# Performance work log

Hardware: AMD Instinct MI355X
Metric: run time of the kernel (lower is better)

## Reference

```python
import jax, jax.numpy as jnp
import numpy as np

B, H_TRAJ, S = 8, 16, 64
DIM, C = 128, 2000
D = 2 * DIM            # transformer d_model
NUM_HEADS, WINDOW, L = 4, 4, 2
D_FF = 4 * D


def setup_inputs() -> dict:
    key = jax.random.key(0)
    ks = jax.random.split(key, 12)
    w = lambda k, shape, s: jax.random.normal(k, shape, jnp.float32) * s
    return {
        "history": jax.random.randint(ks[0], (B, H_TRAJ, S), 0, C + 1),
        "current_trajectory": jax.random.randint(ks[1], (B, S), 0, C + 1),
        "embedding": w(ks[2], (1, C, DIM), 1.0),
        "null_embedding": jax.random.uniform(ks[3], (D,), jnp.float32),
        "gcn_w": w(ks[4], (DIM, DIM), 0.05),
        "gcn_b": jnp.zeros((DIM,), jnp.float32),
        "enc_attn_w": w(ks[5], (L, 4, D, D), 0.05),
        "enc_attn_b": jnp.zeros((L, 4, D), jnp.float32),
        "enc_ffn_w1": w(ks[6], (L, D, D_FF), 0.05),
        "enc_ffn_b1": jnp.zeros((L, D_FF), jnp.float32),
        "enc_ffn_w2": w(ks[7], (L, D_FF, D), 0.05),
        "enc_ffn_b2": jnp.zeros((L, D), jnp.float32),
        "enc_ln_s": jnp.ones((L, 2, D), jnp.float32),
        "enc_ln_b": jnp.zeros((L, 2, D), jnp.float32),
        "wca_w": w(ks[8], (4, D, D), 0.05),
        "wca_b": jnp.zeros((4, D), jnp.float32),
        "ial_w": w(ks[9], (D, DIM), 0.05),
        "ial_b": jnp.zeros((DIM,), jnp.float32),
    }


def _layer_norm(x, s, b, eps=1e-5):
    m = x.mean(-1, keepdims=True)
    v = ((x - m) ** 2).mean(-1, keepdims=True)
    return (x - m) * jax.lax.rsqrt(v + eps) * s + b


def _mha(xq, xkv, w, b, mask):
    # w: (4,d,d) q/k/v/out, b: (4,d); mask additive, broadcast over heads
    d = xq.shape[-1]
    hd = d // NUM_HEADS
    proj = lambda x, i: (x @ w[i] + b[i]).reshape(x.shape[:-1] + (NUM_HEADS, hd))
    q, k, v = proj(xq, 0), proj(xkv, 1), proj(xkv, 2)
    s = jnp.einsum('bqhd,bkhd->bhqk', q, k) / float(np.sqrt(hd))
    s = s + mask[:, None, :, :]
    a = jax.nn.softmax(s, axis=-1)
    o = jnp.einsum('bhqk,bkhd->bqhd', a, v).reshape(xq.shape)
    return o @ w[3] + b[3]


def _get_graph(history):
    # vectorized scatter-add replacement of the python triple loop
    src, dst = history[:, :, :-1], history[:, :, 1:]
    h_idx = jnp.arange(H_TRAJ, dtype=jnp.float32)
    wts = 1.0 + jnp.exp(-0.01 * (H_TRAJ - 1 - h_idx))          # per-trajectory weight
    valid = (src != C) & (dst != C) & (src != dst)
    wv = jnp.where(valid, wts[None, :, None], 0.0)
    sc, dc = jnp.clip(src, 0, C - 1), jnp.clip(dst, 0, C - 1)
    flat = (jnp.arange(B)[:, None, None] * C * C + sc * C + dc).ravel()
    A = jnp.zeros((B * C * C,), jnp.float32).at[flat].add(wv.ravel())
    return A.reshape(B, C, C)


def _mytransform(A):
    A = A + jnp.eye(C, dtype=A.dtype)
    d = jnp.sqrt(A.sum(axis=1))          # torch code: sqrt of dim-1 sums (no inverse)
    return d[:, :, None] * A * d[:, None, :]   # D @ A @ D


def _temporal(seq_len, d):
    t = jnp.arange(seq_len, dtype=jnp.float32)[:, None]
    den = 10000.0 ** (jnp.arange(0, d, 2, dtype=jnp.float32) / d)
    arg = t / den[None, :]
    return jnp.stack([jnp.sin(arg), jnp.cos(arg)], axis=-1).reshape(seq_len, d)


def _fuse(pos, hist, temp, null_emb):
    # pos: (B,C,D); hist: (B,...,S); gather + where fusion
    g = jax.vmap(lambda p, h: p[h])(pos, jnp.clip(hist, 0, C - 1))
    return jnp.where((hist == C)[..., None], null_emb + temp, g + temp)


def _encoder(x, mask, aw, ab, fw1, fb1, fw2, fb2, lns, lnb):
    for l in range(L):
        a = _mha(x, x, aw[l], ab[l], mask)
        x = _layer_norm(x + a, lns[l, 0], lnb[l, 0])
        f = jax.nn.relu(x @ fw1[l] + fb1[l]) @ fw2[l] + fb2[l]
        x = _layer_norm(x + f, lns[l, 1], lnb[l, 1])
    return x


def reference(history, current_trajectory, embedding, null_embedding, gcn_w, gcn_b,
              enc_attn_w, enc_attn_b, enc_ffn_w1, enc_ffn_b1, enc_ffn_w2, enc_ffn_b2,
              enc_ln_s, enc_ln_b, wca_w, wca_b, ial_w, ial_b):
    E = jnp.broadcast_to(embedding, (B, C, DIM))
    A = _mytransform(_get_graph(history))                      # (B,C,C)
    Eg = jax.nn.relu(A @ E @ gcn_w + gcn_b)                    # GCN layer
    pos = jnp.concatenate([E, Eg], axis=-1)                    # (B,C,2*dim)
    temp = _temporal(S, D)
    fh = _fuse(pos, history, temp, null_embedding).reshape(B * H_TRAJ, S, D)
    fc = _fuse(pos, current_trajectory, temp, null_embedding)  # (B,S,D)
    hmask = jnp.broadcast_to(
        jnp.where((history == C)[:, :, None, :], -jnp.inf, 0.0),
        (B, H_TRAJ, S, S)).reshape(B * H_TRAJ, S, S)
    cmask = jnp.broadcast_to(
        jnp.where((current_trajectory == C)[:, None, :], -jnp.inf, 0.0), (B, S, S))
    mh = _encoder(fh, hmask, enc_attn_w, enc_attn_b, enc_ffn_w1, enc_ffn_b1,
                  enc_ffn_w2, enc_ffn_b2, enc_ln_s, enc_ln_b)
    mc = _encoder(fc, cmask, enc_attn_w, enc_attn_b, enc_ffn_w1, enc_ffn_b1,
                  enc_ffn_w2, enc_ffn_b2, enc_ln_s, enc_ln_b)
    cur_rep = jnp.broadcast_to(mc[:, None], (B, H_TRAJ, S, D)).reshape(B * H_TRAJ, S, D)
    i = jnp.arange(S)
    wmask = jnp.where(jnp.abs(i[:, None] - i[None, :]) <= WINDOW, 0.0, -jnp.inf)[None]
    wca = mh + _mha(mh, cur_rep, wca_w, wca_b, wmask)          # window-based cross attn
    wca = wca.reshape(B, H_TRAJ, S, D)
    # information aggregation over the trajectory axis
    scores = jnp.einsum('bhsd,bsd->bhs', wca, mc) / float(np.sqrt(D))
    aw = jax.nn.softmax(scores, axis=1)
    agg = jnp.einsum('bhs,bhsd->bsd', aw, wca)
    final = jax.nn.relu((agg + mc) @ ial_w + ial_b)            # (B,S,dim)
    return final @ embedding[0].T                              # (B,S,C)
```

## Files before the change

kernel.cpp:

```cpp
#include <hip/hip_runtime.h>
#include <hip/hip_bf16.h>
#include <math.h>

#define C_N   2000
#define DIMN  128
#define DM    256
#define B_N   8
#define HT    16
#define S_N   64
#define NSEQ  136
#define DFF   1024
#define NEDGE (B_N*HT*(S_N-1))

typedef __hip_bfloat16 bf16;
typedef short bf16x8 __attribute__((ext_vector_type(8)));
typedef float f32x4  __attribute__((ext_vector_type(4)));

#define GLOAD_LDS16(gp, lp) \
    __builtin_amdgcn_global_load_lds((const __attribute__((address_space(1))) void*)(gp), \
                                     (__attribute__((address_space(3))) void*)(lp), 16, 0, 0)

__device__ __forceinline__ short f2bf(float v) {
    bf16 t = (bf16)v;
    return *reinterpret_cast<short*>(&t);
}


__global__ void k_initX(const float* __restrict__ cs, const float* __restrict__ Y,
                        const float* __restrict__ gb, float* __restrict__ Eg) {
    size_t i = (size_t)blockIdx.x * 256 + threadIdx.x;
    int k = (int)(i % DIMN); size_t bc = i / DIMN;
    int c = (int)(bc % C_N); int b = (int)(bc / C_N);
    float dd2 = 1.f + cs[b * C_N + c];
    Eg[i] = dd2 * Y[(size_t)c * DIMN + k] + gb[k];
}

__global__ void k_edgeX(const int* __restrict__ hist, const float* __restrict__ cs,
                        const float* __restrict__ Y, float* __restrict__ Eg) {
    int e = blockIdx.x;
    int s = e % (S_N-1); int bh = e / (S_N-1); int h = bh % HT; int b = bh / HT;
    const int* row = hist + (size_t)bh * S_N;
    int src = row[s], dst = row[s+1];
    if (src == C_N || dst == C_N || src == dst) return;
    float w = (1.f + expf(-0.01f * (float)(HT - 1 - h)))
            * sqrtf(1.f + cs[b*C_N+src]) * sqrtf(1.f + cs[b*C_N+dst]);
    int k = threadIdx.x;
    atomicAdd(&Eg[((size_t)b * C_N + src) * DIMN + k], w * Y[(size_t)dst * DIMN + k]);
}

struct TEnt { const float* s; bf16* d; int K; int N; int nm; int tiles; };
struct PrepArgs {
    TEnt e[6];
    const float* emb; bf16* embbf;
    const int* hist; float* colsum;
    float* temp;
};

__global__ void k_prep(PrepArgs p) {
    int id = blockIdx.x;
    int t = threadIdx.y * 32 + threadIdx.x;
    if (id < 1840) {
        __shared__ float tl[32][33];
        TEnt en = p.e[0];
        #pragma unroll
        for (int k = 0; k < 6; ++k) {
            if (id < p.e[k].tiles) { en = p.e[k]; break; }
            id -= p.e[k].tiles;
        }
        int tn = en.N >> 5;
        int per = (en.K >> 5) * tn;
        int mat = id / per, t2 = id % per;
        int ty = t2 / tn, tx = t2 % tn;
        const float* s = en.s + (size_t)mat * en.K * en.N;
        bf16* d = en.d + (size_t)mat * en.N * en.K;
        int k0 = ty * 32, n0 = tx * 32;
        #pragma unroll
        for (int j = 0; j < 32; j += 8)
            tl[threadIdx.y + j][threadIdx.x] = s[(size_t)(k0 + threadIdx.y + j) * en.N + n0 + threadIdx.x];
        __syncthreads();
        #pragma unroll
        for (int j = 0; j < 32; j += 8)
            d[(size_t)(n0 + threadIdx.y + j) * en.K + k0 + threadIdx.x] = (bf16)tl[threadIdx.x][threadIdx.y + j];
        return;
    }
    id -= 1840;
    if (id < 250) {
        int i = (id * 256 + t) * 4;
        float4 v = *(const float4*)(p.emb + i);
        bf16* d = p.embbf;
        d[i] = (bf16)v.x; d[i+1] = (bf16)v.y; d[i+2] = (bf16)v.z; d[i+3] = (bf16)v.w;
        return;
    }
    id -= 250;
    if (id < 32) {
        int e = id * 256 + t;
        if (e >= NEDGE) return;
        int s = e % (S_N-1); int bh = e / (S_N-1); int h = bh % HT; int b = bh / HT;
        const int* row = p.hist + (size_t)bh * S_N;
        int src = row[s], dst = row[s+1];
        if (src != C_N && dst != C_N && src != dst) {
            float w = 1.f + expf(-0.01f * (float)(HT - 1 - h));
            atomicAdd(&p.colsum[b * C_N + dst], w);
        }
        return;
    }
    id -= 32;
    {
        int s = id; int d = t;
        int k = d >> 1;
        float den = powf(10000.f, (2.f * (float)k) / 256.f);
        float arg = (float)s / den;
        p.temp[s * DM + d] = (d & 1) ? cosf(arg) : sinf(arg);
    }
}

template<int EPI>
__global__ __launch_bounds__(256) void k_bgemm(
        const bf16* __restrict__ A, const bf16* __restrict__ Bt,
        const float* __restrict__ bias, const float* __restrict__ resid,
        void* __restrict__ Cout, int M, int N, int K, int ldc, int nreal)
{
    __shared__ bf16 As[2][128 * 64];
    __shared__ bf16 Bs[2][64 * 64];
    int tid = threadIdx.x;
    int wid = tid >> 6, lane = tid & 63;
    int m0 = blockIdx.y * 128, n0 = blockIdx.x * 64;
    int wr = wid >> 1, wc = wid & 1;
    int lr = lane >> 3, lc = lane & 7;
    int gc = lc ^ lr;
    f32x4 acc[4][2] = {};
    int nkt = K >> 6;

#define STAGE_BG(kt, buf) { \
    int kb = (kt) << 6; \
    _Pragma("unroll") \
    for (int s = 0; s < 4; ++s) { \
        int seg = wid * 4 + s; int row = seg * 8 + lr; \
        GLOAD_LDS16(A + (size_t)(m0 + row) * K + kb + gc * 8, &As[buf][seg * 512]); \
    } \
    _Pragma("unroll") \
    for (int s = 0; s < 2; ++s) { \
        int seg = wid * 2 + s; int row = seg * 8 + lr; \
        GLOAD_LDS16(Bt + (size_t)(n0 + row) * K + kb + gc * 8, &Bs[buf][seg * 512]); \
    } }

    STAGE_BG(0, 0);
    __syncthreads();
    int cur = 0;
    for (int kt = 0; kt < nkt; ++kt) {
        if (kt + 1 < nkt) STAGE_BG(kt + 1, cur ^ 1);
        #pragma unroll
        for (int kk = 0; kk < 2; ++kk) {
            bf16x8 af[4], bfr[2];
            int c = kk * 4 + (lane >> 4);
            #pragma unroll
            for (int m = 0; m < 4; ++m) {
                int row = wr * 64 + m * 16 + (lane & 15);
                af[m] = *(const bf16x8*)(&As[cur][row * 64 + (c ^ (row & 7)) * 8]);
            }
            #pragma unroll
            for (int n = 0; n < 2; ++n) {
                int row = wc * 32 + n * 16 + (lane & 15);
                bfr[n] = *(const bf16x8*)(&Bs[cur][row * 64 + (c ^ (row & 7)) * 8]);
            }
            #pragma unroll
            for (int m = 0; m < 4; ++m)
                #pragma unroll
                for (int n = 0; n < 2; ++n)
                    acc[m][n] = __builtin_amdgcn_mfma_f32_16x16x32_bf16(af[m], bfr[n], acc[m][n], 0, 0, 0);
        }
        __syncthreads();
        cur ^= 1;
    }
#undef STAGE_BG
    int cl = lane & 15, ch = lane >> 4;
    #pragma unroll
    for (int n = 0; n < 2; ++n) {
        int col = n0 + wc * 32 + n * 16 + cl;
        if ((EPI & 16) && col >= nreal) continue;
        float bv = (EPI & 1) ? bias[col] : 0.f;
        #pragma unroll
        for (int m = 0; m < 4; ++m) {
            #pragma unroll
            for (int j = 0; j < 4; ++j) {
                int row = m0 + wr * 64 + m * 16 + ch * 4 + j;
                float v = acc[m][n][j] + bv;
                if (EPI & 4) v += resid[(size_t)row * ldc + col];
                if (EPI & 2) v = fmaxf(v, 0.f);
                if (EPI & 8) ((bf16*)Cout)[(size_t)row * ldc + col] = (bf16)v;
                else         ((float*)Cout)[(size_t)row * ldc + col] = v;
            }
        }
    }
}

__global__ __launch_bounds__(256) void k_bgemm_ln(
        const bf16* __restrict__ A, const bf16* __restrict__ Bt,
        const float* __restrict__ bias, float* __restrict__ Xf,
        const float* __restrict__ lns_, const float* __restrict__ lnb_,
        bf16* __restrict__ Xb, int M, int K)
{
    __shared__ bf16 As[2][32 * 64];
    __shared__ bf16 Bs[2][256 * 64];
    __shared__ float ls1[32][4], ls2[32][4];
    int tid = threadIdx.x, wid = tid >> 6, lane = tid & 63;
    int lr = lane >> 3, lc = lane & 7, gc = lc ^ lr;
    int cl = lane & 15, ch = lane >> 4;
    int m0 = blockIdx.x * 32;
    int wc = wid;
    f32x4 acc[2][4] = {};
    int nkt = K >> 6;

#define STAGE_LN(kt, buf) { \
    int kb = (kt) << 6; \
    { int row = wid * 8 + lr; \
      GLOAD_LDS16(A + (size_t)(m0 + row) * K + kb + gc * 8, &As[buf][wid * 512]); } \
    _Pragma("unroll") \
    for (int s = 0; s < 8; ++s) { \
        int seg = wid * 8 + s; int row = seg * 8 + lr; \
        GLOAD_LDS16(Bt + (size_t)row * K + kb + gc * 8, &Bs[buf][seg * 512]); \
    } }

    STAGE_LN(0, 0);
    __syncthreads();
    int cur = 0;
    for (int kt = 0; kt < nkt; ++kt) {
        if (kt + 1 < nkt) STAGE_LN(kt + 1, cur ^ 1);
        #pragma unroll
        for (int kk = 0; kk < 2; ++kk) {
            int c = kk * 4 + ch;
            bf16x8 af[2], bfr[4];
            #pragma unroll
            for (int m = 0; m < 2; ++m) {
                int row = m * 16 + cl;
                af[m] = *(const bf16x8*)(&As[cur][row * 64 + (c ^ (row & 7)) * 8]);
            }
            #pragma unroll
            for (int n = 0; n < 4; ++n) {
                int row = wc * 64 + n * 16 + cl;
                bfr[n] = *(const bf16x8*)(&Bs[cur][row * 64 + (c ^ (row & 7)) * 8]);
            }
            #pragma unroll
            for (int m = 0; m < 2; ++m)
                #pragma unroll
                for (int n = 0; n < 4; ++n)
                    acc[m][n] = __builtin_amdgcn_mfma_f32_16x16x32_bf16(af[m], bfr[n], acc[m][n], 0, 0, 0);
        }
        __syncthreads();
        cur ^= 1;
    }
#undef STAGE_LN
    #pragma unroll
    for (int m = 0; m < 2; ++m) {
        #pragma unroll
        for (int j = 0; j < 4; ++j) {
            int rl = m * 16 + ch * 4 + j;
            float s1 = 0.f, s2 = 0.f;
            #pragma unroll
            for (int n = 0; n < 4; ++n) {
                int col = wc * 64 + n * 16 + cl;
                float v = acc[m][n][j] + bias[col] + Xf[(size_t)(m0 + rl) * 256 + col];
                acc[m][n][j] = v;
                s1 += v; s2 += v * v;
            }
            s1 += __shfl_xor(s1, 1); s2 += __shfl_xor(s2, 1);
            s1 += __shfl_xor(s1, 2); s2 += __shfl_xor(s2, 2);
            s1 += __shfl_xor(s1, 4); s2 += __shfl_xor(s2, 4);
            s1 += __shfl_xor(s1, 8); s2 += __shfl_xor(s2, 8);
            if (cl == 0) { ls1[rl][wc] = s1; ls2[rl][wc] = s2; }
        }
    }
    __syncthreads();
    #pragma unroll
    for (int m = 0; m < 2; ++m) {
        #pragma unroll
        for (int j = 0; j < 4; ++j) {
            int rl = m * 16 + ch * 4 + j;
            float su = ls1[rl][0] + ls1[rl][1] + ls1[rl][2] + ls1[rl][3];
            float sq = ls2[rl][0] + ls2[rl][1] + ls2[rl][2] + ls2[rl][3];
            float mean = su * (1.f / 256.f);
            float var  = sq * (1.f / 256.f) - mean * mean;
            float rstd = rsqrtf(var + 1e-5f);
            #pragma unroll
            for (int n = 0; n < 4; ++n) {
                int col = wc * 64 + n * 16 + cl;
                float r = (acc[m][n][j] - mean) * rstd * lns_[col] + lnb_[col];
                size_t g = (size_t)(m0 + rl) * 256 + col;
                Xf[g] = r;
                Xb[g] = (bf16)r;
            }
        }
    }
}


__global__ void k_fuse(const int* __restrict__ hist, const int* __restrict__ cur,
                       const float* __restrict__ E, const float* __restrict__ Eg,
                       const float* __restrict__ nullE, const float* __restrict__ temp,
                       float* __restrict__ Xenc, bf16* __restrict__ Xbf,
                       float* __restrict__ maskb) {
    int blk = blockIdx.x;
    int seq = blk >> 6, s = blk & 63;
    int d = threadIdx.x;
    int idx, b;
    if (seq < 128) { b = seq >> 4; idx = hist[(size_t)seq * S_N + s]; }
    else           { b = seq - 128; idx = cur[b * S_N + s]; }
    float t = temp[s * DM + d];
    float v;
    if (idx == C_N) v = nullE[d] + t;
    else {
        v = ((d < DIMN) ? E[(size_t)idx * DIMN + d]
                        : fmaxf(Eg[((size_t)b * C_N + idx) * DIMN + (d - DIMN)], 0.f)) + t;
    }
    size_t o = ((size_t)seq * S_N + s) * DM + d;
    Xenc[o] = v;
    Xbf[o]  = (bf16)v;
    if (d == 0) maskb[seq * S_N + s] = (idx == C_N) ? -INFINITY : 0.f;
}

template<bool WCA>
__global__ __launch_bounds__(64) void k_mattn(
        const bf16* __restrict__ Qb, const bf16* __restrict__ Kb,
        const bf16* __restrict__ Vb, const float* __restrict__ maskb,
        bf16* __restrict__ O, int qstr, int kstr)
{
    int seq = blockIdx.x >> 2, head = blockIdx.x & 3;
    int lane = threadIdx.x;
    int cl = lane & 15, ch = lane >> 4;
    __shared__ __align__(16) short VT[64 * 72];
    __shared__ __align__(16) short PT[64 * 72];

    const bf16* Qp = Qb + (size_t)seq * 64 * qstr + head * 64;
    int kvseq = WCA ? (seq >> 4) : seq;
    const bf16* Kp = Kb + (size_t)kvseq * 64 * kstr + head * 64;
    const bf16* Vp = Vb + (size_t)kvseq * 64 * kstr + head * 64;

    bf16x8 aq[4][2], bk[4][2], vr[4][2];
    #pragma unroll
    for (int t = 0; t < 4; ++t)
        #pragma unroll
        for (int kk = 0; kk < 2; ++kk) {
            int row = t * 16 + cl, d0 = kk * 32 + ch * 8;
            aq[t][kk] = *(const bf16x8*)(Qp + (size_t)row * qstr + d0);
            bk[t][kk] = *(const bf16x8*)(Kp + (size_t)row * kstr + d0);
            vr[t][kk] = *(const bf16x8*)(Vp + (size_t)row * kstr + d0);
        }

    f32x4 sa[4][4] = {};
    #pragma unroll
    for (int kk = 0; kk < 2; ++kk)
        #pragma unroll
        for (int m = 0; m < 4; ++m)
            #pragma unroll
            for (int n = 0; n < 4; ++n)
                sa[m][n] = __builtin_amdgcn_mfma_f32_16x16x32_bf16(aq[m][kk], bk[n][kk], sa[m][n], 0, 0, 0);

    #pragma unroll
    for (int t = 0; t < 4; ++t)
        #pragma unroll
        for (int kk = 0; kk < 2; ++kk) {
            int k = t * 16 + cl, d0 = kk * 32 + ch * 8;
            #pragma unroll
            for (int e = 0; e < 8; ++e)
                VT[(d0 + e) * 72 + k] = vr[t][kk][e];
        }

    float mk4[4];
    if (!WCA) {
        #pragma unroll
        for (int n = 0; n < 4; ++n) mk4[n] = maskb[seq * 64 + n * 16 + cl];
    }

    #pragma unroll
    for (int m = 0; m < 4; ++m) {
        #pragma unroll
        for (int j = 0; j < 4; ++j) {
            int q = m * 16 + ch * 4 + j;
            float rm = -INFINITY;
            #pragma unroll
            for (int n = 0; n < 4; ++n) {
                int k = n * 16 + cl;
                float msk = WCA ? ((abs(q - k) <= 4) ? 0.f : -INFINITY) : mk4[n];
                float v = sa[m][n][j] * 0.125f + msk;
                sa[m][n][j] = v;
                rm = fmaxf(rm, v);
            }
            rm = fmaxf(rm, __shfl_xor(rm, 1));
            rm = fmaxf(rm, __shfl_xor(rm, 2));
            rm = fmaxf(rm, __shfl_xor(rm, 4));
            rm = fmaxf(rm, __shfl_xor(rm, 8));
            float rs = 0.f;
            #pragma unroll
            for (int n = 0; n < 4; ++n) {
                float e = expf(sa[m][n][j] - rm);
                sa[m][n][j] = e;
                rs += e;
            }
            rs += __shfl_xor(rs, 1);
            rs += __shfl_xor(rs, 2);
            rs += __shfl_xor(rs, 4);
            rs += __shfl_xor(rs, 8);
            float inv = 1.f / rs;
            #pragma unroll
            for (int n = 0; n < 4; ++n)
                PT[q * 72 + n * 16 + cl] = f2bf(sa[m][n][j] * inv);
        }
    }
    __syncthreads();

    f32x4 oa[4][4] = {};
    #pragma unroll
    for (int kk = 0; kk < 2; ++kk) {
        bf16x8 av[4], bp[4];
        #pragma unroll
        for (int dm = 0; dm < 4; ++dm)
            av[dm] = *(const bf16x8*)(VT + (dm * 16 + cl) * 72 + kk * 32 + ch * 8);
        #pragma unroll
        for (int qn = 0; qn < 4; ++qn)
            bp[qn] = *(const bf16x8*)(PT + (qn * 16 + cl) * 72 + kk * 32 + ch * 8);
        #pragma unroll
        for (int dm = 0; dm < 4; ++dm)
            #pragma unroll
            for (int qn = 0; qn < 4; ++qn)
                oa[dm][qn] = __builtin_amdgcn_mfma_f32_16x16x32_bf16(av[dm], bp[qn], oa[dm][qn], 0, 0, 0);
    }
    __syncthreads();

    #pragma unroll
    for (int dm = 0; dm < 4; ++dm)
        #pragma unroll
        for (int qn = 0; qn < 4; ++qn)
            #pragma unroll
            for (int j = 0; j < 4; ++j)
                PT[(qn * 16 + cl) * 72 + dm * 16 + ch * 4 + j] = f2bf(oa[dm][qn][j]);
    __syncthreads();
    #pragma unroll
    for (int it = 0; it < 8; ++it) {
        int chunk = it * 64 + lane;
        int tok = chunk >> 3, d0 = (chunk & 7) * 8;
        bf16x8 v = *(const bf16x8*)(PT + tok * 72 + d0);
        *(bf16x8*)(O + ((size_t)seq * 64 + tok) * 256 + head * 64 + d0) = v;
    }
}


__global__ __launch_bounds__(256) void k_agg(const float* __restrict__ wca,
                                             const float* __restrict__ mc,
                                             bf16* __restrict__ aggbf) {
    int bs = blockIdx.x; int b = bs >> 6, s = bs & 63;
    int d = threadIdx.x;
    __shared__ float red[4][16];
    float mcv = mc[((size_t)b * S_N + s) * DM + d];
    float wv[16], p[16];
    #pragma unroll
    for (int h = 0; h < 16; ++h) {
        wv[h] = wca[(((size_t)(b * HT + h)) * S_N + s) * DM + d];
        p[h] = wv[h] * mcv;
    }
    #pragma unroll
    for (int o = 1; o < 64; o <<= 1)
        #pragma unroll
        for (int h = 0; h < 16; ++h) p[h] += __shfl_xor(p[h], o);
    if ((d & 63) == 0) {
        int w = d >> 6;
        #pragma unroll
        for (int h = 0; h < 16; ++h) red[w][h] = p[h];
    }
    __syncthreads();
    float sc[16], mx = -INFINITY;
    #pragma unroll
    for (int h = 0; h < 16; ++h) {
        sc[h] = (red[0][h] + red[1][h] + red[2][h] + red[3][h]) * (1.f / 16.f);
        mx = fmaxf(mx, sc[h]);
    }
    float e[16], sum = 0.f;
    #pragma unroll
    for (int h = 0; h < 16; ++h) { e[h] = expf(sc[h] - mx); sum += e[h]; }
    float inv = 1.f / sum;
    float acc = 0.f;
    #pragma unroll
    for (int h = 0; h < 16; ++h) acc += e[h] * inv * wv[h];
    aggbf[((size_t)b * S_N + s) * DM + d] = (bf16)(acc + mcv);
}


extern "C" void kernel_launch(void* const* d_in, const int* in_sizes, int n_in,
                              void* d_out, int out_size, void* d_ws, size_t ws_size,
                              hipStream_t stream) {
    const int*   history = (const int*)d_in[0];
    const int*   cur     = (const int*)d_in[1];
    const float* emb     = (const float*)d_in[2];
    const float* nullE   = (const float*)d_in[3];
    const float* gcn_w   = (const float*)d_in[4];
    const float* gcn_b   = (const float*)d_in[5];
    const float* aw      = (const float*)d_in[6];
    const float* ab      = (const float*)d_in[7];
    const float* fw1     = (const float*)d_in[8];
    const float* fb1     = (const float*)d_in[9];
    const float* fw2     = (const float*)d_in[10];
    const float* fb2     = (const float*)d_in[11];
    const float* lns     = (const float*)d_in[12];
    const float* lnb     = (const float*)d_in[13];
    const float* wca_w   = (const float*)d_in[14];
    const float* wca_b   = (const float*)d_in[15];
    const float* ial_w   = (const float*)d_in[16];
    const float* ial_b   = (const float*)d_in[17];
    float* out = (float*)d_out;
    float* ws  = (float*)d_ws;

    float* dvec   = ws + 0;
    float* maskb  = ws + 16000;
    float* temp   = ws + 24704;
    bf16*  aggbf  = (bf16*)(ws + 41088);
    bf16*  finalb = (bf16*)(ws + 106624);
    bf16*  embbf  = (bf16*)(ws + 139392);
    float* Y      = ws + 270464;
    float* Eg     = ws + 532608;
    bf16*  wbf    = (bf16*)(ws + 2580608);
    float* Xenc   = ws + 3522688;
    bf16*  Xbf    = (bf16*)(ws + 5750912);
    bf16*  Abf    = (bf16*)(ws + 6865024);
    bf16*  Hbf    = (bf16*)(ws + 7979136);
    bf16*  QKVbf  = (bf16*)(ws + 12435584);
    float* SE     = ws + 15777920;

    bf16* wbf_aw  = wbf;
    bf16* wbf_fw1 = wbf + 524288;
    bf16* wbf_fw2 = wbf + 1048576;
    bf16* wbf_wca = wbf + 1572864;
    bf16* wbf_gcn = wbf + 1835008;
    bf16* wbf_ial = wbf + 1851392;

    bf16* Qwbf = QKVbf;
    bf16* KVbf = QKVbf + 4194304;

    hipMemsetAsync(dvec, 0, 16000 * sizeof(float), stream);
    hipMemsetAsync(embbf + 2000 * 128, 0, 48 * 128 * sizeof(bf16), stream);
    PrepArgs pa;
    pa.e[0] = { aw,    wbf_aw,  256,  256, 8, 512 };
    pa.e[1] = { fw1,   wbf_fw1, 256, 1024, 2, 512 };
    pa.e[2] = { fw2,   wbf_fw2, 1024, 256, 2, 512 };
    pa.e[3] = { wca_w, wbf_wca, 256,  256, 4, 256 };
    pa.e[4] = { gcn_w, wbf_gcn, 128,  128, 1,  16 };
    pa.e[5] = { ial_w, wbf_ial, 256,  128, 1,  32 };
    pa.emb = emb; pa.embbf = embbf;
    pa.hist = history; pa.colsum = dvec;
    pa.temp = temp;
    k_prep<<<1840 + 250 + 32 + 64, dim3(32, 8), 0, stream>>>(pa);

    k_bgemm<0><<<dim3(2, 16), 256, 0, stream>>>(embbf, wbf_gcn, nullptr, nullptr, Y,
                                                2048, DIMN, DIMN, DIMN, DIMN);
    k_initX<<<B_N * C_N * DIMN / 256, 256, 0, stream>>>(dvec, Y, gcn_b, Eg);
    k_edgeX<<<NEDGE, 128, 0, stream>>>(history, dvec, Y, Eg);

    k_fuse<<<NSEQ * S_N, DM, 0, stream>>>(history, cur, emb, Eg, nullE, temp, Xenc, Xbf, maskb);

    for (int l = 0; l < 2; ++l) {
        k_bgemm<9><<<dim3(12, 68), 256, 0, stream>>>(Xbf, wbf_aw + l * 262144,
                ab + l * 1024, nullptr, QKVbf, NSEQ * S_N, 768, 256, 768, 768);
        k_mattn<false><<<NSEQ * 4, 64, 0, stream>>>(QKVbf, QKVbf + 256, QKVbf + 512,
                maskb, Abf, 768, 768);
        k_bgemm_ln<<<272, 256, 0, stream>>>(Abf, wbf_aw + l * 262144 + 196608,
                ab + l * 1024 + 768, Xenc, lns + (l * 2 + 0) * DM, lnb + (l * 2 + 0) * DM,
                Xbf, NSEQ * S_N, 256);
        k_bgemm<11><<<dim3(16, 68), 256, 0, stream>>>(Xbf, wbf_fw1 + l * 262144,
                fb1 + l * DFF, nullptr, Hbf, NSEQ * S_N, DFF, 256, DFF, DFF);
        k_bgemm_ln<<<272, 256, 0, stream>>>(Hbf, wbf_fw2 + l * 262144,
                fb2 + l * DM, Xenc, lns + (l * 2 + 1) * DM, lnb + (l * 2 + 1) * DM,
                Xbf, NSEQ * S_N, 1024);
    }

    float* mh = Xenc;
    bf16*  mc_bf = Xbf + (size_t)128 * S_N * DM;

    k_bgemm<9><<<dim3(4, 64), 256, 0, stream>>>(Xbf, wbf_wca, wca_b, nullptr, Qwbf,
                                                128 * S_N, 256, 256, 256, 256);
    k_bgemm<9><<<dim3(8, 4), 256, 0, stream>>>(mc_bf, wbf_wca + 65536, wca_b + 256, nullptr,
                                               KVbf, B_N * S_N, 512, 256, 512, 512);
    k_mattn<true><<<128 * 4, 64, 0, stream>>>(Qwbf, KVbf, KVbf + 256, nullptr, Abf, 256, 512);
    k_bgemm<5><<<dim3(4, 64), 256, 0, stream>>>(Abf, wbf_wca + 196608, wca_b + 768, mh, SE,
                                                128 * S_N, 256, 256, 256, 256);

    k_agg<<<B_N * S_N, 256, 0, stream>>>(SE, Xenc + (size_t)128 * S_N * DM, aggbf);
    k_bgemm<11><<<dim3(2, 4), 256, 0, stream>>>(aggbf, wbf_ial, ial_b, nullptr, finalb,
                                                B_N * S_N, DIMN, DM, DIMN, DIMN);
    k_bgemm<16><<<dim3(32, 4), 256, 0, stream>>>(finalb, embbf, nullptr, nullptr, out,
                                                 B_N * S_N, 2048, DIMN, C_N, C_N);
}
```

Baseline: 320.7 us.

## Fuse attention with output projection and LayerNorm, widen GEMM tiles to 128x128

Attention now runs one block per sequence with four head warps. The per-head outputs are staged in LDS and multiplied directly by the output-projection weight, followed by the residual add and LayerNorm (or, for the window cross-attention, the residual write into SE). This removes the Abf round trip and one GEMM launch per layer. The generic GEMM tile grows from 128x64 to 128x128, and the cross-attention Q and KV projections are merged into one launch. The trade-off is fewer blocks per launch (136 or 128 for attention) with more LDS per block, so occupancy and parallelism drop.

```diff
diff --git a/kernel.cpp b/kernel.cpp
--- a/kernel.cpp
+++ b/kernel.cpp
@@ -11,6 +11,7 @@
 #define NSEQ  136
 #define DFF   1024
 #define NEDGE (B_N*HT*(S_N-1))
+#define OTS   264
 
 typedef __hip_bfloat16 bf16;
 typedef short bf16x8 __attribute__((ext_vector_type(8)));
@@ -115,68 +116,66 @@
 }
 
 template<int EPI>
-__global__ __launch_bounds__(256) void k_bgemm(
+__device__ __forceinline__ void bgemm2_body(
         const bf16* __restrict__ A, const bf16* __restrict__ Bt,
-        const float* __restrict__ bias, const float* __restrict__ resid,
-        void* __restrict__ Cout, int M, int N, int K, int ldc, int nreal)
+        const float* __restrict__ bias, void* __restrict__ Cout,
+        int m0, int n0, int K, int ldc, int nreal,
+        bf16* __restrict__ As, bf16* __restrict__ Bs)
 {
-    __shared__ bf16 As[2][128 * 64];
-    __shared__ bf16 Bs[2][64 * 64];
     int tid = threadIdx.x;
     int wid = tid >> 6, lane = tid & 63;
-    int m0 = blockIdx.y * 128, n0 = blockIdx.x * 64;
     int wr = wid >> 1, wc = wid & 1;
     int lr = lane >> 3, lc = lane & 7;
     int gc = lc ^ lr;
-    f32x4 acc[4][2] = {};
+    f32x4 acc[4][4] = {};
     int nkt = K >> 6;
 
-#define STAGE_BG(kt, buf) { \
+#define STAGE2(kt, buf) { \
     int kb = (kt) << 6; \
     _Pragma("unroll") \
     for (int s = 0; s < 4; ++s) { \
         int seg = wid * 4 + s; int row = seg * 8 + lr; \
-        GLOAD_LDS16(A + (size_t)(m0 + row) * K + kb + gc * 8, &As[buf][seg * 512]); \
+        GLOAD_LDS16(A + (size_t)(m0 + row) * K + kb + gc * 8, As + (buf) * 8192 + seg * 512); \
     } \
     _Pragma("unroll") \
-    for (int s = 0; s < 2; ++s) { \
-        int seg = wid * 2 + s; int row = seg * 8 + lr; \
-        GLOAD_LDS16(Bt + (size_t)(n0 + row) * K + kb + gc * 8, &Bs[buf][seg * 512]); \
+    for (int s = 0; s < 4; ++s) { \
+        int seg = wid * 4 + s; int row = seg * 8 + lr; \
+        GLOAD_LDS16(Bt + (size_t)(n0 + row) * K + kb + gc * 8, Bs + (buf) * 8192 + seg * 512); \
     } }
 
-    STAGE_BG(0, 0);
+    STAGE2(0, 0);
     __syncthreads();
     int cur = 0;
     for (int kt = 0; kt < nkt; ++kt) {
-        if (kt + 1 < nkt) STAGE_BG(kt + 1, cur ^ 1);
+        if (kt + 1 < nkt) STAGE2(kt + 1, cur ^ 1);
         #pragma unroll
         for (int kk = 0; kk < 2; ++kk) {
-            bf16x8 af[4], bfr[2];
+            bf16x8 af[4], bfr[4];
             int c = kk * 4 + (lane >> 4);
             #pragma unroll
             for (int m = 0; m < 4; ++m) {
                 int row = wr * 64 + m * 16 + (lane & 15);
-                af[m] = *(const bf16x8*)(&As[cur][row * 64 + (c ^ (row & 7)) * 8]);
-            }
-            #pragma unroll
-            for (int n = 0; n < 2; ++n) {
-                int row = wc * 32 + n * 16 + (lane & 15);
-                bfr[n] = *(const bf16x8*)(&Bs[cur][row * 64 + (c ^ (row & 7)) * 8]);
+                af[m] = *(const bf16x8*)(As + cur * 8192 + row * 64 + (c ^ (row & 7)) * 8);
+            }
+            #pragma unroll
+            for (int n = 0; n < 4; ++n) {
+                int row = wc * 64 + n * 16 + (lane & 15);
+                bfr[n] = *(const bf16x8*)(Bs + cur * 8192 + row * 64 + (c ^ (row & 7)) * 8);
             }
             #pragma unroll
             for (int m = 0; m < 4; ++m)
                 #pragma unroll
-                for (int n = 0; n < 2; ++n)
+                for (int n = 0; n < 4; ++n)
                     acc[m][n] = __builtin_amdgcn_mfma_f32_16x16x32_bf16(af[m], bfr[n], acc[m][n], 0, 0, 0);
         }
         __syncthreads();
         cur ^= 1;
     }
-#undef STAGE_BG
+#undef STAGE2
     int cl = lane & 15, ch = lane >> 4;
     #pragma unroll
-    for (int n = 0; n < 2; ++n) {
-        int col = n0 + wc * 32 + n * 16 + cl;
+    for (int n = 0; n < 4; ++n) {
+        int col = n0 + wc * 64 + n * 16 + cl;
         if ((EPI & 16) && col >= nreal) continue;
         float bv = (EPI & 1) ? bias[col] : 0.f;
         #pragma unroll
@@ -185,12 +184,39 @@
             for (int j = 0; j < 4; ++j) {
                 int row = m0 + wr * 64 + m * 16 + ch * 4 + j;
                 float v = acc[m][n][j] + bv;
-                if (EPI & 4) v += resid[(size_t)row * ldc + col];
                 if (EPI & 2) v = fmaxf(v, 0.f);
                 if (EPI & 8) ((bf16*)Cout)[(size_t)row * ldc + col] = (bf16)v;
                 else         ((float*)Cout)[(size_t)row * ldc + col] = v;
             }
         }
+    }
+}
+
+template<int EPI>
+__global__ __launch_bounds__(256) void k_bgemm2(
+        const bf16* __restrict__ A, const bf16* __restrict__ Bt,
+        const float* __restrict__ bias, void* __restrict__ Cout,
+        int K, int ldc, int nreal)
+{
+    __shared__ bf16 As[2][8192], Bs[2][8192];
+    bgemm2_body<EPI>(A, Bt, bias, Cout, blockIdx.y * 128, blockIdx.x * 128,
+                     K, ldc, nreal, &As[0][0], &Bs[0][0]);
+}
+
+__global__ __launch_bounds__(256) void k_wcaqkv(
+        const bf16* __restrict__ Xbf, const bf16* __restrict__ mcbf,
+        const bf16* __restrict__ wwca, const float* __restrict__ wb,
+        bf16* __restrict__ Q, bf16* __restrict__ KV)
+{
+    __shared__ bf16 As[2][8192], Bs[2][8192];
+    int bid = blockIdx.x;
+    if (bid < 128)
+        bgemm2_body<9>(Xbf, wwca, wb, Q, (bid >> 1) * 128, (bid & 1) * 128,
+                       256, 256, 0, &As[0][0], &Bs[0][0]);
+    else {
+        int l = bid - 128;
+        bgemm2_body<9>(mcbf, wwca + 65536, wb + 256, KV, (l >> 2) * 128, (l & 3) * 128,
+                       256, 512, 0, &As[0][0], &Bs[0][0]);
     }
 }
 
@@ -319,17 +345,28 @@
 }
 
 template<bool WCA>
-__global__ __launch_bounds__(64) void k_mattn(
+__global__ __launch_bounds__(256) void k_attnfuse(
         const bf16* __restrict__ Qb, const bf16* __restrict__ Kb,
         const bf16* __restrict__ Vb, const float* __restrict__ maskb,
-        bf16* __restrict__ O, int qstr, int kstr)
+        const bf16* __restrict__ Wt, const float* __restrict__ bias,
+        float* __restrict__ Xf, const float* __restrict__ lns_,
+        const float* __restrict__ lnb_, bf16* __restrict__ Xb,
+        float* __restrict__ SEout)
 {
-    int seq = blockIdx.x >> 2, head = blockIdx.x & 3;
-    int lane = threadIdx.x;
+    int seq = blockIdx.x;
+    int tid = threadIdx.x;
+    int wid = tid >> 6, lane = tid & 63;
+    int head = wid;
     int cl = lane & 15, ch = lane >> 4;
-    __shared__ __align__(16) short VT[64 * 72];
-    __shared__ __align__(16) short PT[64 * 72];
-
+    __shared__ __align__(16) short VTall[4][64 * 72];
+    __shared__ __align__(16) short PTall[4][64 * 72];
+    __shared__ __align__(16) short OT[64 * OTS];
+    __shared__ float ls1[64][4], ls2[64][4];
+    short* VT = VTall[wid];
+    short* PT = PTall[wid];
+
+    const int qstr = WCA ? 256 : 768;
+    const int kstr = WCA ? 512 : 768;
     const bf16* Qp = Qb + (size_t)seq * 64 * qstr + head * 64;
     int kvseq = WCA ? (seq >> 4) : seq;
     const bf16* Kp = Kb + (size_t)kvseq * 64 * kstr + head * 64;
@@ -345,7 +382,6 @@
             bk[t][kk] = *(const bf16x8*)(Kp + (size_t)row * kstr + d0);
             vr[t][kk] = *(const bf16x8*)(Vp + (size_t)row * kstr + d0);
         }
-
     f32x4 sa[4][4] = {};
     #pragma unroll
     for (int kk = 0; kk < 2; ++kk)
@@ -354,7 +390,6 @@
             #pragma unroll
             for (int n = 0; n < 4; ++n)
                 sa[m][n] = __builtin_amdgcn_mfma_f32_16x16x32_bf16(aq[m][kk], bk[n][kk], sa[m][n], 0, 0, 0);
-
     #pragma unroll
     for (int t = 0; t < 4; ++t)
         #pragma unroll
@@ -364,13 +399,11 @@
             for (int e = 0; e < 8; ++e)
                 VT[(d0 + e) * 72 + k] = vr[t][kk][e];
         }
-
     float mk4[4];
     if (!WCA) {
         #pragma unroll
         for (int n = 0; n < 4; ++n) mk4[n] = maskb[seq * 64 + n * 16 + cl];
     }
-
     #pragma unroll
     for (int m = 0; m < 4; ++m) {
         #pragma unroll
@@ -406,8 +439,6 @@
                 PT[q * 72 + n * 16 + cl] = f2bf(sa[m][n][j] * inv);
         }
     }
-    __syncthreads();
-
     f32x4 oa[4][4] = {};
     #pragma unroll
     for (int kk = 0; kk < 2; ++kk) {
@@ -424,22 +455,91 @@
             for (int qn = 0; qn < 4; ++qn)
                 oa[dm][qn] = __builtin_amdgcn_mfma_f32_16x16x32_bf16(av[dm], bp[qn], oa[dm][qn], 0, 0, 0);
     }
+    #pragma unroll
+    for (int dm = 0; dm < 4; ++dm)
+        #pragma unroll
+        for (int qn = 0; qn < 4; ++qn)
+            #pragma unroll
+            for (int j = 0; j < 4; ++j)
+                OT[(qn * 16 + cl) * OTS + head * 64 + dm * 16 + ch * 4 + j] = f2bf(oa[dm][qn][j]);
     __syncthreads();
 
-    #pragma unroll
-    for (int dm = 0; dm < 4; ++dm)
-        #pragma unroll
-        for (int qn = 0; qn < 4; ++qn)
-            #pragma unroll
-            for (int j = 0; j < 4; ++j)
-                PT[(qn * 16 + cl) * 72 + dm * 16 + ch * 4 + j] = f2bf(oa[dm][qn][j]);
+    f32x4 acc[4][4] = {};
+    #pragma unroll 2
+    for (int kt = 0; kt < 8; ++kt) {
+        int k0 = kt * 32 + ch * 8;
+        bf16x8 af[4], bfr[4];
+        #pragma unroll
+        for (int m = 0; m < 4; ++m)
+            af[m] = *(const bf16x8*)(OT + (m * 16 + cl) * OTS + k0);
+        #pragma unroll
+        for (int n = 0; n < 4; ++n) {
+            int col = wid * 64 + n * 16 + cl;
+            bfr[n] = *(const bf16x8*)(Wt + (size_t)col * 256 + k0);
+        }
+        #pragma unroll
+        for (int m = 0; m < 4; ++m)
+            #pragma unroll
+            for (int n = 0; n < 4; ++n)
+                acc[m][n] = __builtin_amdgcn_mfma_f32_16x16x32_bf16(af[m], bfr[n], acc[m][n], 0, 0, 0);
+    }
+
+    if (WCA) {
+        #pragma unroll
+        for (int m = 0; m < 4; ++m)
+            #pragma unroll
+            for (int j = 0; j < 4; ++j) {
+                int rl = m * 16 + ch * 4 + j;
+                size_t rb = ((size_t)seq * 64 + rl) * 256;
+                #pragma unroll
+                for (int n = 0; n < 4; ++n) {
+                    int col = wid * 64 + n * 16 + cl;
+                    SEout[rb + col] = acc[m][n][j] + bias[col] + Xf[rb + col];
+                }
+            }
+        return;
+    }
+    #pragma unroll
+    for (int m = 0; m < 4; ++m) {
+        #pragma unroll
+        for (int j = 0; j < 4; ++j) {
+            int rl = m * 16 + ch * 4 + j;
+            size_t rb = ((size_t)seq * 64 + rl) * 256;
+            float s1 = 0.f, s2 = 0.f;
+            #pragma unroll
+            for (int n = 0; n < 4; ++n) {
+                int col = wid * 64 + n * 16 + cl;
+                float v = acc[m][n][j] + bias[col] + Xf[rb + col];
+                acc[m][n][j] = v;
+                s1 += v; s2 += v * v;
+            }
+            s1 += __shfl_xor(s1, 1); s2 += __shfl_xor(s2, 1);
+            s1 += __shfl_xor(s1, 2); s2 += __shfl_xor(s2, 2);
+            s1 += __shfl_xor(s1, 4); s2 += __shfl_xor(s2, 4);
+            s1 += __shfl_xor(s1, 8); s2 += __shfl_xor(s2, 8);
+            if (cl == 0) { ls1[rl][wid] = s1; ls2[rl][wid] = s2; }
+        }
+    }
     __syncthreads();
     #pragma unroll
-    for (int it = 0; it < 8; ++it) {
-        int chunk = it * 64 + lane;
-        int tok = chunk >> 3, d0 = (chunk & 7) * 8;
-        bf16x8 v = *(const bf16x8*)(PT + tok * 72 + d0);
-        *(bf16x8*)(O + ((size_t)seq * 64 + tok) * 256 + head * 64 + d0) = v;
+    for (int m = 0; m < 4; ++m) {
+        #pragma unroll
+        for (int j = 0; j < 4; ++j) {
+            int rl = m * 16 + ch * 4 + j;
+            float su = ls1[rl][0] + ls1[rl][1] + ls1[rl][2] + ls1[rl][3];
+            float sq = ls2[rl][0] + ls2[rl][1] + ls2[rl][2] + ls2[rl][3];
+            float mean = su * (1.f / 256.f);
+            float var  = sq * (1.f / 256.f) - mean * mean;
+            float rstd = rsqrtf(var + 1e-5f);
+            size_t rb = ((size_t)seq * 64 + rl) * 256;
+            #pragma unroll
+            for (int n = 0; n < 4; ++n) {
+                int col = wid * 64 + n * 16 + cl;
+                float r = (acc[m][n][j] - mean) * rstd * lns_[col] + lnb_[col];
+                Xf[rb + col] = r;
+                Xb[rb + col] = (bf16)r;
+            }
+        }
     }
 }
 
@@ -519,10 +619,9 @@
     bf16*  wbf    = (bf16*)(ws + 2580608);
     float* Xenc   = ws + 3522688;
     bf16*  Xbf    = (bf16*)(ws + 5750912);
-    bf16*  Abf    = (bf16*)(ws + 6865024);
-    bf16*  Hbf    = (bf16*)(ws + 7979136);
-    bf16*  QKVbf  = (bf16*)(ws + 12435584);
-    float* SE     = ws + 15777920;
+    bf16*  Hbf    = (bf16*)(ws + 6865024);
+    bf16*  QKVbf  = (bf16*)(ws + 11321472);
+    float* SE     = ws + 14663808;
 
     bf16* wbf_aw  = wbf;
     bf16* wbf_fw1 = wbf + 524288;
@@ -548,23 +647,20 @@
     pa.temp = temp;
     k_prep<<<1840 + 250 + 32 + 64, dim3(32, 8), 0, stream>>>(pa);
 
-    k_bgemm<0><<<dim3(2, 16), 256, 0, stream>>>(embbf, wbf_gcn, nullptr, nullptr, Y,
-                                                2048, DIMN, DIMN, DIMN, DIMN);
+    k_bgemm2<0><<<dim3(1, 16), 256, 0, stream>>>(embbf, wbf_gcn, nullptr, Y, DIMN, DIMN, 0);
     k_initX<<<B_N * C_N * DIMN / 256, 256, 0, stream>>>(dvec, Y, gcn_b, Eg);
     k_edgeX<<<NEDGE, 128, 0, stream>>>(history, dvec, Y, Eg);
 
     k_fuse<<<NSEQ * S_N, DM, 0, stream>>>(history, cur, emb, Eg, nullE, temp, Xenc, Xbf, maskb);
 
     for (int l = 0; l < 2; ++l) {
-        k_bgemm<9><<<dim3(12, 68), 256, 0, stream>>>(Xbf, wbf_aw + l * 262144,
-                ab + l * 1024, nullptr, QKVbf, NSEQ * S_N, 768, 256, 768, 768);
-        k_mattn<false><<<NSEQ * 4, 64, 0, stream>>>(QKVbf, QKVbf + 256, QKVbf + 512,
-                maskb, Abf, 768, 768);
-        k_bgemm_ln<<<272, 256, 0, stream>>>(Abf, wbf_aw + l * 262144 + 196608,
-                ab + l * 1024 + 768, Xenc, lns + (l * 2 + 0) * DM, lnb + (l * 2 + 0) * DM,
-                Xbf, NSEQ * S_N, 256);
-        k_bgemm<11><<<dim3(16, 68), 256, 0, stream>>>(Xbf, wbf_fw1 + l * 262144,
-                fb1 + l * DFF, nullptr, Hbf, NSEQ * S_N, DFF, 256, DFF, DFF);
+        k_bgemm2<9><<<dim3(6, 68), 256, 0, stream>>>(Xbf, wbf_aw + l * 262144,
+                ab + l * 1024, QKVbf, 256, 768, 0);
+        k_attnfuse<false><<<NSEQ, 256, 0, stream>>>(QKVbf, QKVbf + 256, QKVbf + 512,
+                maskb, wbf_aw + l * 262144 + 196608, ab + l * 1024 + 768,
+                Xenc, lns + (l * 2 + 0) * DM, lnb + (l * 2 + 0) * DM, Xbf, nullptr);
+        k_bgemm2<11><<<dim3(8, 68), 256, 0, stream>>>(Xbf, wbf_fw1 + l * 262144,
+                fb1 + l * DFF, Hbf, 256, DFF, 0);
         k_bgemm_ln<<<272, 256, 0, stream>>>(Hbf, wbf_fw2 + l * 262144,
                 fb2 + l * DM, Xenc, lns + (l * 2 + 1) * DM, lnb + (l * 2 + 1) * DM,
                 Xbf, NSEQ * S_N, 1024);
@@ -573,17 +669,11 @@
     float* mh = Xenc;
     bf16*  mc_bf = Xbf + (size_t)128 * S_N * DM;
 
-    k_bgemm<9><<<dim3(4, 64), 256, 0, stream>>>(Xbf, wbf_wca, wca_b, nullptr, Qwbf,
-                                                128 * S_N, 256, 256, 256, 256);
-    k_bgemm<9><<<dim3(8, 4), 256, 0, stream>>>(mc_bf, wbf_wca + 65536, wca_b + 256, nullptr,
-                                               KVbf, B_N * S_N, 512, 256, 512, 512);
-    k_mattn<true><<<128 * 4, 64, 0, stream>>>(Qwbf, KVbf, KVbf + 256, nullptr, Abf, 256, 512);
-    k_bgemm<5><<<dim3(4, 64), 256, 0, stream>>>(Abf, wbf_wca + 196608, wca_b + 768, mh, SE,
-                                                128 * S_N, 256, 256, 256, 256);
+    k_wcaqkv<<<144, 256, 0, stream>>>(Xbf, mc_bf, wbf_wca, wca_b, Qwbf, KVbf);
+    k_attnfuse<true><<<128, 256, 0, stream>>>(Qwbf, KVbf, KVbf + 256, nullptr,
+            wbf_wca + 196608, wca_b + 768, mh, nullptr, nullptr, nullptr, SE);
 
     k_agg<<<B_N * S_N, 256, 0, stream>>>(SE, Xenc + (size_t)128 * S_N * DM, aggbf);
-    k_bgemm<11><<<dim3(2, 4), 256, 0, stream>>>(aggbf, wbf_ial, ial_b, nullptr, finalb,
-                                                B_N * S_N, DIMN, DM, DIMN, DIMN);
-    k_bgemm<16><<<dim3(32, 4), 256, 0, stream>>>(finalb, embbf, nullptr, nullptr, out,
-                                                 B_N * S_N, 2048, DIMN, C_N, C_N);
-}
+    k_bgemm2<11><<<dim3(1, 4), 256, 0, stream>>>(aggbf, wbf_ial, ial_b, finalb, DM, DIMN, 0);
+    k_bgemm2<16><<<dim3(16, 4), 256, 0, stream>>>(finalb, embbf, nullptr, out, DIMN, C_N, C_N);
+}
```

Measured after the change: 322.2 us. No clear change (+0.5%).
